# Kernel tuning notes

Hardware: AMD Instinct MI355X
Metric: run time of the kernel (lower is better)

Reference implementation:

```python
import jax, jax.numpy as jnp
import numpy as np

E = 512        # embed_dim
H = 16         # num_heads
R = 8          # num_relation_heads
NH = H - R     # num_normal_heads
HD = E // H    # head_dim
SCALING = HD ** -0.5
B, LQ, LK = 2, 2048, 2048


def setup_inputs() -> dict:
    key = jax.random.key(0)
    ks = jax.random.split(key, 14)
    s = 1.0 / np.sqrt(E)  # keep pre-softmax logits moderate so exp() is stable
    inp = {
        "query": jax.random.normal(ks[0], (B, LQ, E), jnp.float32),
        "key": jax.random.normal(ks[1], (B, LK, E), jnp.float32),
        "value": jax.random.normal(ks[2], (B, LK, E), jnp.float32),
        "relation_weights": jax.random.uniform(ks[3], (B, R, LQ, LK), jnp.float32),
        "Wq": jax.random.normal(ks[4], (E, E), jnp.float32) * s,
        "bq": jnp.zeros((E,), jnp.float32),
        "Wk": jax.random.normal(ks[5], (E, E), jnp.float32) * s,
        "bk": jnp.zeros((E,), jnp.float32),
        "Wv": jax.random.normal(ks[6], (E, E), jnp.float32) * s,
        "bv": jnp.zeros((E,), jnp.float32),
        "Wo": jax.random.normal(ks[7], (E, E), jnp.float32) * s,
        "bo": jnp.zeros((E,), jnp.float32),
        "ln_gamma": jnp.ones((E,), jnp.float32),
        "ln_beta": jnp.zeros((E,), jnp.float32),
    }
    return inp


def reference(query, key, value, relation_weights, Wq, bq, Wk, bk, Wv, bv, Wo, bo, ln_gamma, ln_beta):
    b, lq, _ = query.shape
    lk = key.shape[1]
    # projections; weights stored as [in, out] so y = x @ W + b
    q = (query @ Wq + bq).reshape(b, lq, H, HD)
    k = (key @ Wk + bk).reshape(b, lk, H, HD)
    v = (value @ Wv + bv).reshape(b, lk, H, HD)
    # scores: [B, H, Lq, Lk]
    scores = jnp.einsum("bqhd,bkhd->bhqk", q, k) * SCALING
    # normal heads: standard softmax
    normal_attn = jax.nn.softmax(scores[:, :NH], axis=-1)
    # relation heads: exp(scores) * relation_weights, renormalized
    rel = jnp.exp(scores[:, NH:]) * relation_weights
    rel = rel / (rel.sum(axis=-1, keepdims=True) + 1e-6)
    attn = jnp.concatenate([normal_attn, rel], axis=1)  # [B, H, Lq, Lk]
    # weighted values -> [B, Lq, E]
    out = jnp.einsum("bhqk,bkhd->bqhd", attn, v).reshape(b, lq, E)
    out = out @ Wo + bo
    # LayerNorm (eps=1e-5, torch default)
    mu = out.mean(axis=-1, keepdims=True)
    var = out.var(axis=-1, keepdims=True)
    out = (out - mu) * jax.lax.rsqrt(var + 1e-5) * ln_gamma + ln_beta
    return out
```

## Files before the change

### kernel.cpp

```cpp
#include <hip/hip_runtime.h>


using u16 = unsigned short;
using u32 = unsigned int;

typedef __attribute__((ext_vector_type(8))) short bf16x8;
typedef __attribute__((ext_vector_type(8))) _Float16 f16x8;
typedef __attribute__((ext_vector_type(4))) float f32x4;

#define H_  16
#define NH_ 8
#define HD_ 32
#define L_  2048
#define E_  512
#define B_  2
#define M_  4096
#define KSPLIT 2
static constexpr float QSCALE_ = 0.17677669529663689f * 1.44269504088896340f;

__device__ inline u16 f2bf(float x) {
  union { float f; u32 u; } v; v.f = x;
  u32 r = v.u + 0x7FFFu + ((v.u >> 16) & 1u);
  return (u16)(r >> 16);
}
__device__ inline float bf2f(u16 x) {
  union { u32 u; float f; } v; v.u = ((u32)x) << 16; return v.f;
}
__device__ inline u16 f2h(float x) {
  union { _Float16 h; u16 u; } v; v.h = (_Float16)x; return v.u;
}
__device__ inline float h2f(u16 x) {
  union { u16 u; _Float16 h; } v; v.u = x; return (float)v.h;
}

__global__ __launch_bounds__(256) void k_prep(const float* __restrict__ qa, const float* __restrict__ ka,
                                              const float* __restrict__ va,
                                              u16* __restrict__ oq, u16* __restrict__ ok, u16* __restrict__ ov,
                                              const float* __restrict__ Wq, const float* __restrict__ Wk,
                                              const float* __restrict__ Wv, const float* __restrict__ Wo,
                                              u16* __restrict__ Tq, u16* __restrict__ Tk,
                                              u16* __restrict__ Tv, u16* __restrict__ To) {
  __shared__ u16 tile[64][65];
  int y = blockIdx.y;
  if (y < 3) {
    const float* s = (y == 0) ? qa : (y == 1) ? ka : va;
    u16* d = (y == 0) ? oq : (y == 1) ? ok : ov;
    size_t i = ((size_t)blockIdx.x * 256 + threadIdx.x) * 4;
    float4 v = *(const float4*)(s + i);
    uint2 pk;
    pk.x = (u32)f2bf(v.x) | ((u32)f2bf(v.y) << 16);
    pk.y = (u32)f2bf(v.z) | ((u32)f2bf(v.w) << 16);
    *(uint2*)(d + i) = pk;
    return;
  }
  if (blockIdx.x >= 256) return;
  int bid = blockIdx.x;
  int z = bid >> 6, rem = bid & 63;
  int r0 = ((rem >> 3) & 7) * 64, c0 = (rem & 7) * 64;
  const float* W = (z == 0) ? Wq : (z == 1) ? Wk : (z == 2) ? Wv : Wo;
  u16* T = (z == 0) ? Tq : (z == 1) ? Tk : (z == 2) ? Tv : To;
  int tw = threadIdx.x >> 6, tl = threadIdx.x & 63;
#pragma unroll
  for (int i = 0; i < 16; ++i) {
    int r = i * 4 + tw;
    tile[r][tl] = f2bf(W[(size_t)(r0 + r) * E_ + c0 + tl]);
  }
  __syncthreads();
#pragma unroll
  for (int i = 0; i < 16; ++i) {
    int r = i * 4 + tw;
    T[(size_t)(c0 + r) * E_ + r0 + tl] = tile[tl][r];
  }
}

template <int MODE>
__device__ inline void gemm_body(const u16* __restrict__ A, const u16* __restrict__ Bt,
                                 const float* __restrict__ bias, void* __restrict__ out,
                                 const float* __restrict__ pden, float oscale, int ofmt) {
  __shared__ __align__(16) u16 smem[2 * 64 * 72];
  u16* As = smem;
  u16* Bs = smem + 64 * 72;
  const int tid = threadIdx.x;
  const int lane = tid & 63, wid = tid >> 6;
  const int m0 = blockIdx.x * 64, n0 = blockIdx.y * 64;
  const int wm = (wid >> 1) * 32, wn = (wid & 1) * 32;
  const int mrow = lane & 15, quad = lane >> 4;
  f32x4 acc[2][2] = {};
  for (int k0 = 0; k0 < 512; k0 += 64) {
    __syncthreads();
#pragma unroll
    for (int i = 0; i < 2; ++i) {
      int task = i * 256 + tid;
      int r = task >> 3, c = task & 7;
      *(uint4*)(Bs + r * 72 + c * 8) = *(const uint4*)(Bt + (size_t)(n0 + r) * 512 + k0 + c * 8);
      if (MODE == 0) {
        *(uint4*)(As + r * 72 + c * 8) = *(const uint4*)(A + (size_t)(m0 + r) * 512 + k0 + c * 8);
      } else {
        int gm = m0 + r;
        int bb = gm >> 11, q = gm & (L_ - 1);
        int e0 = k0 + c * 8;
        int hh = e0 >> 5, d = e0 & (HD_ - 1);
        size_t i0 = ((size_t)(0 * B_ + bb) * H_ + hh) * L_ + q;
        size_t i1 = ((size_t)(1 * B_ + bb) * H_ + hh) * L_ + q;
        uint4 n0v = *(const uint4*)(A + i0 * HD_ + d);
        uint4 n1v = *(const uint4*)(A + i1 * HD_ + d);
        float den = pden[i0] + pden[i1] + ((hh >= NH_) ? 1e-6f : 0.f);
        float rinv = __builtin_amdgcn_rcpf(den);
        const u16* p0 = (const u16*)&n0v;
        const u16* p1 = (const u16*)&n1v;
        u16 o8[8];
#pragma unroll
        for (int j = 0; j < 8; ++j) o8[j] = f2bf((h2f(p0[j]) + h2f(p1[j])) * rinv);
        *(uint4*)(As + r * 72 + c * 8) = *(const uint4*)o8;
      }
    }
    __syncthreads();
#pragma unroll
    for (int kk = 0; kk < 64; kk += 32) {
      bf16x8 af[2], bfr[2];
#pragma unroll
      for (int f = 0; f < 2; ++f)
        af[f] = *(const bf16x8*)(As + (wm + f * 16 + mrow) * 72 + kk + quad * 8);
#pragma unroll
      for (int f = 0; f < 2; ++f)
        bfr[f] = *(const bf16x8*)(Bs + (wn + f * 16 + mrow) * 72 + kk + quad * 8);
#pragma unroll
      for (int fm = 0; fm < 2; ++fm)
#pragma unroll
        for (int fn = 0; fn < 2; ++fn)
          acc[fm][fn] = __builtin_amdgcn_mfma_f32_16x16x32_bf16(af[fm], bfr[fn], acc[fm][fn], 0, 0, 0);
    }
  }
  if (MODE == 0) {
    __syncthreads();
    u16* wscr = smem + wid * (32 * 36);
#pragma unroll
    for (int fn = 0; fn < 2; ++fn) {
      float bv = bias[n0 + wn + fn * 16 + mrow];
#pragma unroll
      for (int fm = 0; fm < 2; ++fm)
#pragma unroll
        for (int r = 0; r < 4; ++r) {
          float x = (acc[fm][fn][r] + bv) * oscale;
          wscr[(fm * 16 + quad * 4 + r) * 36 + fn * 16 + mrow] = ofmt ? f2h(x) : f2bf(x);
        }
    }
    asm volatile("s_waitcnt lgkmcnt(0)" ::: "memory");
    const int hg = (n0 + wn) >> 5;
    const int row = lane >> 1, j = lane & 1;
    int gm = m0 + wm + row;
    int bb = gm >> 11, q = gm & (L_ - 1);
    u16* dst = (u16*)out + (((size_t)(bb * H_ + hg)) * L_ + q) * HD_ + j * 16;
    uint4 v0 = *(const uint4*)(wscr + row * 36 + j * 16);
    uint4 v1 = *(const uint4*)(wscr + row * 36 + j * 16 + 8);
    *(uint4*)dst = v0;
    *(uint4*)(dst + 8) = v1;
  } else {
#pragma unroll
    for (int fn = 0; fn < 2; ++fn) {
      int gn = n0 + wn + fn * 16 + mrow;
      float bv = bias[gn];
#pragma unroll
      for (int fm = 0; fm < 2; ++fm)
#pragma unroll
        for (int r = 0; r < 4; ++r) {
          int gm = m0 + wm + fm * 16 + quad * 4 + r;
          ((float*)out)[(size_t)gm * E_ + gn] = acc[fm][fn][r] + bv;
        }
    }
  }
}

__global__ __launch_bounds__(256) void k_gemm_qkv(const u16* Xq, const u16* Xk, const u16* Xv,
                                                  const u16* Tq, const u16* Tk, const u16* Tv,
                                                  const float* bq, const float* bk, const float* bv,
                                                  u16* Qb, u16* Kb, u16* Vb) {
  int z = blockIdx.z;
  const u16* A = (z == 0) ? Xq : (z == 1) ? Xk : Xv;
  const u16* T = (z == 0) ? Tq : (z == 1) ? Tk : Tv;
  const float* bi = (z == 0) ? bq : (z == 1) ? bk : bv;
  u16* o = (z == 0) ? Qb : (z == 1) ? Kb : Vb;
  float os = (z == 0) ? QSCALE_ : 1.0f;
  int of = (z == 2) ? 1 : 0;
  gemm_body<0>(A, T, bi, o, nullptr, os, of);
}

__global__ __launch_bounds__(256) void k_gemm_o(const u16* Pnum, const u16* T, const float* bi,
                                                float* Y, const float* Pden) {
  gemm_body<1>(Pnum, T, bi, Y, Pden, 1.0f, 0);
}

__global__ __launch_bounds__(256) void k_attn(const u16* __restrict__ Qb, const u16* __restrict__ Kb,
                                              const u16* __restrict__ Vb, const float* __restrict__ relw,
                                              u16* __restrict__ Pnum, float* __restrict__ Pden) {
  const int tid = threadIdx.x, lane = tid & 63, wid = tid >> 6;
  const int lid = blockIdx.x + 32 * blockIdx.y + 512 * blockIdx.z;
  const int xcd = lid & 7, rest = lid >> 3;
  const int qb = rest & 31, ghi = rest >> 5;
  const int g = ghi * 8 + xcd;
  const int h = g & 15, zz = g >> 4;
  const int b = zz & 1, s = zz >> 1;
  const int q0 = qb * 64;
  const int kbase = s * (L_ / KSPLIT);
  const int kend = kbase + L_ / KSPLIT;
  const bool isrel = (h >= NH_);
  const size_t headOff = ((size_t)(b * H_ + h)) * L_ * HD_;
  const float* wbase = isrel ? relw + ((size_t)(b * (H_ - NH_) + (h - NH_))) * L_ * L_ : nullptr;

  __shared__ __align__(16) u16 Qs[64 * 40];
  __shared__ __align__(16) u16 Ks[64 * 40];
  __shared__ __align__(16) u16 Vts[32 * 72];
  __shared__ __align__(16) u16 Ps[4][16 * 72];
  __shared__ __align__(16) u16 Ws[64 * 68];

  {
    int r = tid >> 2, c = tid & 3;
    *(uint4*)(Qs + r * 40 + c * 8) = *(const uint4*)(Qb + headOff + (size_t)(q0 + r) * HD_ + c * 8);
  }
  __syncthreads();
  const int mrow = lane & 15, quad = lane >> 4;
  bf16x8 qa = *(const bf16x8*)(Qs + (wid * 16 + mrow) * 40 + quad * 8);
  f32x4 accd[2] = {};
  float den[4] = {0.f, 0.f, 0.f, 0.f};

  uint4 rA, rB;
  float4 rw[4];
  const int vp = tid >> 2, vc = tid & 3;
  const int t2 = tid - 128;
  const int wq = tid >> 2, wkc = (tid & 3) * 4;

  auto LOAD = [&](int kt) {
    if (tid < 128) {
      const u16* vsrc = Vb + headOff + (size_t)(kt + 2 * vp) * HD_ + vc * 8;
      rA = *(const uint4*)(vsrc);
      rB = *(const uint4*)(vsrc + HD_);
    } else {
      int task0 = t2 * 2, task1 = t2 * 2 + 1;
      rA = *(const uint4*)(Kb + headOff + (size_t)(kt + (task0 >> 2)) * HD_ + (task0 & 3) * 8);
      rB = *(const uint4*)(Kb + headOff + (size_t)(kt + (task1 >> 2)) * HD_ + (task1 & 3) * 8);
    }
    if (isrel) {
      const float* wsrc = wbase + (size_t)(q0 + wq) * L_ + kt + wkc;
#pragma unroll
      for (int j = 0; j < 4; ++j) rw[j] = *(const float4*)(wsrc + j * 16);
    }
  };
  auto WRITE = [&]() {
    if (tid < 128) {
      const u16* s0 = (const u16*)&rA;
      const u16* s1 = (const u16*)&rB;
#pragma unroll
      for (int i = 0; i < 8; ++i) {
        u32 pk = (u32)s0[i] | ((u32)s1[i] << 16);
        *(u32*)(Vts + (vc * 8 + i) * 72 + 2 * vp) = pk;
      }
    } else {
      int task0 = t2 * 2, task1 = t2 * 2 + 1;
      *(uint4*)(Ks + (task0 >> 2) * 40 + (task0 & 3) * 8) = rA;
      *(uint4*)(Ks + (task1 >> 2) * 40 + (task1 & 3) * 8) = rB;
    }
    if (isrel) {
#pragma unroll
      for (int j = 0; j < 4; ++j) {
        uint2 pk;
        pk.x = (u32)f2bf(rw[j].x) | ((u32)f2bf(rw[j].y) << 16);
        pk.y = (u32)f2bf(rw[j].z) | ((u32)f2bf(rw[j].w) << 16);
        *(uint2*)(Ws + wq * 68 + wkc + j * 16) = pk;
      }
    }
  };

  LOAD(kbase);
  for (int kt = kbase; kt < kend; kt += 64) {
    __syncthreads();
    WRITE();
    if (kt + 64 < kend) LOAD(kt + 64);
    __syncthreads();

    u16* pw = Ps[wid];
#pragma unroll
    for (int f = 0; f < 4; ++f) {
      bf16x8 kb = *(const bf16x8*)(Ks + (f * 16 + mrow) * 40 + quad * 8);
      f32x4 z = {0.f, 0.f, 0.f, 0.f};
      f32x4 sc = __builtin_amdgcn_mfma_f32_16x16x32_bf16(qa, kb, z, 0, 0, 0);
#pragma unroll
      for (int r = 0; r < 4; ++r) {
        float e = exp2f(sc[r]);
        if (isrel)
          e *= bf2f(Ws[(wid * 16 + quad * 4 + r) * 68 + f * 16 + mrow]);
        den[r] += e;
        pw[(quad * 4 + r) * 72 + f * 16 + mrow] = f2h(e);
      }
    }
    asm volatile("s_waitcnt lgkmcnt(0)" ::: "memory");
#pragma unroll
    for (int kk = 0; kk < 2; ++kk) {
      f16x8 pa = *(const f16x8*)(pw + mrow * 72 + kk * 32 + quad * 8);
#pragma unroll
      for (int dh = 0; dh < 2; ++dh) {
        f16x8 vhf = *(const f16x8*)(Vts + (dh * 16 + mrow) * 72 + kk * 32 + quad * 8);
        accd[dh] = __builtin_amdgcn_mfma_f32_16x16x32_f16(pa, vhf, accd[dh], 0, 0, 0);
      }
    }
  }

#pragma unroll
  for (int off = 1; off < 16; off <<= 1)
#pragma unroll
    for (int r = 0; r < 4; ++r) den[r] += __shfl_xor(den[r], off, 64);

  const size_t pidx = ((size_t)(s * B_ + b) * H_ + h) * L_;
#pragma unroll
  for (int dh = 0; dh < 2; ++dh)
#pragma unroll
    for (int r = 0; r < 4; ++r) {
      int qg = q0 + wid * 16 + quad * 4 + r;
      Pnum[(pidx + qg) * HD_ + dh * 16 + mrow] = f2h(accd[dh][r]);
    }
  if (mrow == 0) {
    int qg = q0 + wid * 16 + quad * 4;
    float4 dv = {den[0], den[1], den[2], den[3]};
    *(float4*)(Pden + pidx + qg) = dv;
  }
}

__global__ __launch_bounds__(256) void k_ln(const float* __restrict__ Y, const float* __restrict__ gamma,
                                            const float* __restrict__ beta, float* __restrict__ out) {
  int row = blockIdx.x, tid = threadIdx.x;
  const float* y = Y + (size_t)row * E_;
  float2 v = *(const float2*)(y + tid * 2);
  float s = v.x + v.y, sq = v.x * v.x + v.y * v.y;
#pragma unroll
  for (int off = 1; off < 64; off <<= 1) {
    s += __shfl_xor(s, off, 64);
    sq += __shfl_xor(sq, off, 64);
  }
  __shared__ float ss[4], ssq[4];
  int wid = tid >> 6, lane = tid & 63;
  if (lane == 0) { ss[wid] = s; ssq[wid] = sq; }
  __syncthreads();
  s = ss[0] + ss[1] + ss[2] + ss[3];
  sq = ssq[0] + ssq[1] + ssq[2] + ssq[3];
  float mean = s * (1.f / E_);
  float var = sq * (1.f / E_) - mean * mean;
  float rstd = rsqrtf(var + 1e-5f);
  float2 g = *(const float2*)(gamma + tid * 2);
  float2 be = *(const float2*)(beta + tid * 2);
  float2 o;
  o.x = (v.x - mean) * rstd * g.x + be.x;
  o.y = (v.y - mean) * rstd * g.y + be.y;
  *(float2*)(out + (size_t)row * E_ + tid * 2) = o;
}

extern "C" void kernel_launch(void* const* d_in, const int* in_sizes, int n_in,
                              void* d_out, int out_size, void* d_ws, size_t ws_size,
                              hipStream_t stream) {
  const float* query = (const float*)d_in[0];
  const float* key   = (const float*)d_in[1];
  const float* value = (const float*)d_in[2];
  const float* relw  = (const float*)d_in[3];
  const float* Wq = (const float*)d_in[4];
  const float* bq = (const float*)d_in[5];
  const float* Wk = (const float*)d_in[6];
  const float* bk = (const float*)d_in[7];
  const float* Wv = (const float*)d_in[8];
  const float* bv = (const float*)d_in[9];
  const float* Wo = (const float*)d_in[10];
  const float* bo = (const float*)d_in[11];
  const float* gamma = (const float*)d_in[12];
  const float* beta  = (const float*)d_in[13];

  char* ws = (char*)d_ws;
  u16* Xq = (u16*)(ws + 0);
  u16* Xk = (u16*)(ws + 4194304);
  u16* Xv = (u16*)(ws + 8388608);
  u16* Tq = (u16*)(ws + 12582912);
  u16* Tk = (u16*)(ws + 13107200);
  u16* Tv = (u16*)(ws + 13631488);
  u16* To = (u16*)(ws + 14155776);
  u16* Qb = (u16*)(ws + 14680064);
  u16* Kb = (u16*)(ws + 18874368);
  u16* Vb = (u16*)(ws + 23068672);
  u16*   Pnum = (u16*)(ws + 0);
  float* Pden = (float*)(ws + 8388608);
  float* Y = (float*)(ws + 14680064);

  k_prep<<<dim3(2048, 4, 1), 256, 0, stream>>>(query, key, value, Xq, Xk, Xv,
                                               Wq, Wk, Wv, Wo, Tq, Tk, Tv, To);
  k_gemm_qkv<<<dim3(64, 8, 3), 256, 0, stream>>>(Xq, Xk, Xv, Tq, Tk, Tv, bq, bk, bv, Qb, Kb, Vb);
  k_attn<<<dim3(32, 16, B_ * KSPLIT), 256, 0, stream>>>(Qb, Kb, Vb, relw, Pnum, Pden);
  k_gemm_o<<<dim3(64, 8, 1), 256, 0, stream>>>(Pnum, To, bo, Y, Pden);
  k_ln<<<M_, 256, 0, stream>>>(Y, gamma, beta, (float*)d_out);
}
```

Before: 478.0 us.

## Drop split-K attention, fuse input bf16 cast into QKV GEMM, normalize in-kernel

```diff
diff --git a/kernel.cpp b/kernel.cpp
--- a/kernel.cpp
+++ b/kernel.cpp
@@ -15,7 +15,6 @@
 #define E_  512
 #define B_  2
 #define M_  4096
-#define KSPLIT 2
 static constexpr float QSCALE_ = 0.17677669529663689f * 1.44269504088896340f;
 
 __device__ inline u16 f2bf(float x) {
@@ -23,42 +22,19 @@
   u32 r = v.u + 0x7FFFu + ((v.u >> 16) & 1u);
   return (u16)(r >> 16);
 }
-__device__ inline float bf2f(u16 x) {
-  union { u32 u; float f; } v; v.u = ((u32)x) << 16; return v.f;
-}
 __device__ inline u16 f2h(float x) {
   union { _Float16 h; u16 u; } v; v.h = (_Float16)x; return v.u;
 }
-__device__ inline float h2f(u16 x) {
-  union { u16 u; _Float16 h; } v; v.u = x; return (float)v.h;
-}
-
-__global__ __launch_bounds__(256) void k_prep(const float* __restrict__ qa, const float* __restrict__ ka,
-                                              const float* __restrict__ va,
-                                              u16* __restrict__ oq, u16* __restrict__ ok, u16* __restrict__ ov,
-                                              const float* __restrict__ Wq, const float* __restrict__ Wk,
-                                              const float* __restrict__ Wv, const float* __restrict__ Wo,
-                                              u16* __restrict__ Tq, u16* __restrict__ Tk,
-                                              u16* __restrict__ Tv, u16* __restrict__ To) {
-  __shared__ u16 tile[64][65];
-  int y = blockIdx.y;
-  if (y < 3) {
-    const float* s = (y == 0) ? qa : (y == 1) ? ka : va;
-    u16* d = (y == 0) ? oq : (y == 1) ? ok : ov;
-    size_t i = ((size_t)blockIdx.x * 256 + threadIdx.x) * 4;
-    float4 v = *(const float4*)(s + i);
-    uint2 pk;
-    pk.x = (u32)f2bf(v.x) | ((u32)f2bf(v.y) << 16);
-    pk.y = (u32)f2bf(v.z) | ((u32)f2bf(v.w) << 16);
-    *(uint2*)(d + i) = pk;
-    return;
-  }
-  if (blockIdx.x >= 256) return;
-  int bid = blockIdx.x;
-  int z = bid >> 6, rem = bid & 63;
-  int r0 = ((rem >> 3) & 7) * 64, c0 = (rem & 7) * 64;
+
+__global__ __launch_bounds__(256) void k_wtrans(const float* __restrict__ Wq, const float* __restrict__ Wk,
+                                                const float* __restrict__ Wv, const float* __restrict__ Wo,
+                                                u16* __restrict__ Tq, u16* __restrict__ Tk,
+                                                u16* __restrict__ Tv, u16* __restrict__ To) {
+  int z = blockIdx.z;
   const float* W = (z == 0) ? Wq : (z == 1) ? Wk : (z == 2) ? Wv : Wo;
   u16* T = (z == 0) ? Tq : (z == 1) ? Tk : (z == 2) ? Tv : To;
+  __shared__ u16 tile[64][65];
+  int r0 = blockIdx.y * 64, c0 = blockIdx.x * 64;
   int tw = threadIdx.x >> 6, tl = threadIdx.x & 63;
 #pragma unroll
   for (int i = 0; i < 16; ++i) {
@@ -73,10 +49,10 @@
   }
 }
 
-template <int MODE>
-__device__ inline void gemm_body(const u16* __restrict__ A, const u16* __restrict__ Bt,
+template <int AF32, int EPI>
+__device__ inline void gemm_body(const void* __restrict__ A, const u16* __restrict__ Bt,
                                  const float* __restrict__ bias, void* __restrict__ out,
-                                 const float* __restrict__ pden, float oscale, int ofmt) {
+                                 float oscale, int ofmt) {
   __shared__ __align__(16) u16 smem[2 * 64 * 72];
   u16* As = smem;
   u16* Bs = smem + 64 * 72;
@@ -93,25 +69,16 @@
       int task = i * 256 + tid;
       int r = task >> 3, c = task & 7;
       *(uint4*)(Bs + r * 72 + c * 8) = *(const uint4*)(Bt + (size_t)(n0 + r) * 512 + k0 + c * 8);
-      if (MODE == 0) {
-        *(uint4*)(As + r * 72 + c * 8) = *(const uint4*)(A + (size_t)(m0 + r) * 512 + k0 + c * 8);
+      if (AF32) {
+        const float* af = (const float*)A + (size_t)(m0 + r) * 512 + k0 + c * 8;
+        float4 v0 = *(const float4*)af;
+        float4 v1 = *(const float4*)(af + 4);
+        u16 o8[8] = {f2bf(v0.x), f2bf(v0.y), f2bf(v0.z), f2bf(v0.w),
+                     f2bf(v1.x), f2bf(v1.y), f2bf(v1.z), f2bf(v1.w)};
+        *(uint4*)(As + r * 72 + c * 8) = *(const uint4*)o8;
       } else {
-        int gm = m0 + r;
-        int bb = gm >> 11, q = gm & (L_ - 1);
-        int e0 = k0 + c * 8;
-        int hh = e0 >> 5, d = e0 & (HD_ - 1);
-        size_t i0 = ((size_t)(0 * B_ + bb) * H_ + hh) * L_ + q;
-        size_t i1 = ((size_t)(1 * B_ + bb) * H_ + hh) * L_ + q;
-        uint4 n0v = *(const uint4*)(A + i0 * HD_ + d);
-        uint4 n1v = *(const uint4*)(A + i1 * HD_ + d);
-        float den = pden[i0] + pden[i1] + ((hh >= NH_) ? 1e-6f : 0.f);
-        float rinv = __builtin_amdgcn_rcpf(den);
-        const u16* p0 = (const u16*)&n0v;
-        const u16* p1 = (const u16*)&n1v;
-        u16 o8[8];
-#pragma unroll
-        for (int j = 0; j < 8; ++j) o8[j] = f2bf((h2f(p0[j]) + h2f(p1[j])) * rinv);
-        *(uint4*)(As + r * 72 + c * 8) = *(const uint4*)o8;
+        *(uint4*)(As + r * 72 + c * 8) =
+            *(const uint4*)((const u16*)A + (size_t)(m0 + r) * 512 + k0 + c * 8);
       }
     }
     __syncthreads();
@@ -131,7 +98,7 @@
           acc[fm][fn] = __builtin_amdgcn_mfma_f32_16x16x32_bf16(af[fm], bfr[fn], acc[fm][fn], 0, 0, 0);
     }
   }
-  if (MODE == 0) {
+  if (EPI == 0) {
     __syncthreads();
     u16* wscr = smem + wid * (32 * 36);
 #pragma unroll
@@ -171,65 +138,54 @@
   }
 }
 
-__global__ __launch_bounds__(256) void k_gemm_qkv(const u16* Xq, const u16* Xk, const u16* Xv,
+__global__ __launch_bounds__(256) void k_gemm_qkv(const float* Xq, const float* Xk, const float* Xv,
                                                   const u16* Tq, const u16* Tk, const u16* Tv,
                                                   const float* bq, const float* bk, const float* bv,
                                                   u16* Qb, u16* Kb, u16* Vb) {
   int z = blockIdx.z;
-  const u16* A = (z == 0) ? Xq : (z == 1) ? Xk : Xv;
+  const float* A = (z == 0) ? Xq : (z == 1) ? Xk : Xv;
   const u16* T = (z == 0) ? Tq : (z == 1) ? Tk : Tv;
   const float* bi = (z == 0) ? bq : (z == 1) ? bk : bv;
   u16* o = (z == 0) ? Qb : (z == 1) ? Kb : Vb;
   float os = (z == 0) ? QSCALE_ : 1.0f;
   int of = (z == 2) ? 1 : 0;
-  gemm_body<0>(A, T, bi, o, nullptr, os, of);
-}
-
-__global__ __launch_bounds__(256) void k_gemm_o(const u16* Pnum, const u16* T, const float* bi,
-                                                float* Y, const float* Pden) {
-  gemm_body<1>(Pnum, T, bi, Y, Pden, 1.0f, 0);
+  gemm_body<1, 0>(A, T, bi, o, os, of);
+}
+
+__global__ __launch_bounds__(256) void k_gemm_o(const u16* AO, const u16* T, const float* bi,
+                                                float* Y) {
+  gemm_body<0, 1>(AO, T, bi, Y, 1.0f, 0);
 }
 
 __global__ __launch_bounds__(256) void k_attn(const u16* __restrict__ Qb, const u16* __restrict__ Kb,
                                               const u16* __restrict__ Vb, const float* __restrict__ relw,
-                                              u16* __restrict__ Pnum, float* __restrict__ Pden) {
+                                              u16* __restrict__ AO) {
   const int tid = threadIdx.x, lane = tid & 63, wid = tid >> 6;
   const int lid = blockIdx.x + 32 * blockIdx.y + 512 * blockIdx.z;
   const int xcd = lid & 7, rest = lid >> 3;
   const int qb = rest & 31, ghi = rest >> 5;
   const int g = ghi * 8 + xcd;
-  const int h = g & 15, zz = g >> 4;
-  const int b = zz & 1, s = zz >> 1;
+  const int h = g & 15, b = g >> 4;
   const int q0 = qb * 64;
-  const int kbase = s * (L_ / KSPLIT);
-  const int kend = kbase + L_ / KSPLIT;
   const bool isrel = (h >= NH_);
   const size_t headOff = ((size_t)(b * H_ + h)) * L_ * HD_;
   const float* wbase = isrel ? relw + ((size_t)(b * (H_ - NH_) + (h - NH_))) * L_ * L_ : nullptr;
 
-  __shared__ __align__(16) u16 Qs[64 * 40];
   __shared__ __align__(16) u16 Ks[64 * 40];
   __shared__ __align__(16) u16 Vts[32 * 72];
   __shared__ __align__(16) u16 Ps[4][16 * 72];
-  __shared__ __align__(16) u16 Ws[64 * 68];
-
-  {
-    int r = tid >> 2, c = tid & 3;
-    *(uint4*)(Qs + r * 40 + c * 8) = *(const uint4*)(Qb + headOff + (size_t)(q0 + r) * HD_ + c * 8);
-  }
-  __syncthreads();
+
   const int mrow = lane & 15, quad = lane >> 4;
-  bf16x8 qa = *(const bf16x8*)(Qs + (wid * 16 + mrow) * 40 + quad * 8);
+  bf16x8 qa = *(const bf16x8*)(Qb + headOff + (size_t)(q0 + wid * 16 + mrow) * HD_ + quad * 8);
   f32x4 accd[2] = {};
   float den[4] = {0.f, 0.f, 0.f, 0.f};
 
   uint4 rA, rB;
-  float4 rw[4];
+  float rwv[16];
   const int vp = tid >> 2, vc = tid & 3;
   const int t2 = tid - 128;
-  const int wq = tid >> 2, wkc = (tid & 3) * 4;
-
-  auto LOAD = [&](int kt) {
+
+  auto LOAD_KV = [&](int kt) {
     if (tid < 128) {
       const u16* vsrc = Vb + headOff + (size_t)(kt + 2 * vp) * HD_ + vc * 8;
       rA = *(const uint4*)(vsrc);
@@ -239,10 +195,15 @@
       rA = *(const uint4*)(Kb + headOff + (size_t)(kt + (task0 >> 2)) * HD_ + (task0 & 3) * 8);
       rB = *(const uint4*)(Kb + headOff + (size_t)(kt + (task1 >> 2)) * HD_ + (task1 & 3) * 8);
     }
+  };
+  auto LOAD_REL = [&](int kt) {
     if (isrel) {
-      const float* wsrc = wbase + (size_t)(q0 + wq) * L_ + kt + wkc;
-#pragma unroll
-      for (int j = 0; j < 4; ++j) rw[j] = *(const float4*)(wsrc + j * 16);
+      const float* wsrc = wbase + (size_t)(q0 + wid * 16 + quad * 4) * L_ + kt + mrow;
+#pragma unroll
+      for (int r = 0; r < 4; ++r)
+#pragma unroll
+        for (int f = 0; f < 4; ++f)
+          rwv[r * 4 + f] = wsrc[(size_t)r * L_ + f * 16];
     }
   };
   auto WRITE = [&]() {
@@ -259,22 +220,14 @@
       *(uint4*)(Ks + (task0 >> 2) * 40 + (task0 & 3) * 8) = rA;
       *(uint4*)(Ks + (task1 >> 2) * 40 + (task1 & 3) * 8) = rB;
     }
-    if (isrel) {
-#pragma unroll
-      for (int j = 0; j < 4; ++j) {
-        uint2 pk;
-        pk.x = (u32)f2bf(rw[j].x) | ((u32)f2bf(rw[j].y) << 16);
-        pk.y = (u32)f2bf(rw[j].z) | ((u32)f2bf(rw[j].w) << 16);
-        *(uint2*)(Ws + wq * 68 + wkc + j * 16) = pk;
-      }
-    }
   };
 
-  LOAD(kbase);
-  for (int kt = kbase; kt < kend; kt += 64) {
+  LOAD_KV(0);
+  LOAD_REL(0);
+  for (int kt = 0; kt < L_; kt += 64) {
     __syncthreads();
     WRITE();
-    if (kt + 64 < kend) LOAD(kt + 64);
+    if (kt + 64 < L_) LOAD_KV(kt + 64);
     __syncthreads();
 
     u16* pw = Ps[wid];
@@ -287,11 +240,12 @@
       for (int r = 0; r < 4; ++r) {
         float e = exp2f(sc[r]);
         if (isrel)
-          e *= bf2f(Ws[(wid * 16 + quad * 4 + r) * 68 + f * 16 + mrow]);
+          e *= rwv[r * 4 + f];
         den[r] += e;
         pw[(quad * 4 + r) * 72 + f * 16 + mrow] = f2h(e);
       }
     }
+    if (kt + 64 < L_) LOAD_REL(kt + 64);
     asm volatile("s_waitcnt lgkmcnt(0)" ::: "memory");
 #pragma unroll
     for (int kk = 0; kk < 2; ++kk) {
@@ -309,19 +263,22 @@
 #pragma unroll
     for (int r = 0; r < 4; ++r) den[r] += __shfl_xor(den[r], off, 64);
 
-  const size_t pidx = ((size_t)(s * B_ + b) * H_ + h) * L_;
+  float rinv[4];
+#pragma unroll
+  for (int r = 0; r < 4; ++r)
+    rinv[r] = __builtin_amdgcn_rcpf(den[r] + (isrel ? 1e-6f : 0.f));
+
+  u16* pw = Ps[wid];
 #pragma unroll
   for (int dh = 0; dh < 2; ++dh)
 #pragma unroll
-    for (int r = 0; r < 4; ++r) {
-      int qg = q0 + wid * 16 + quad * 4 + r;
-      Pnum[(pidx + qg) * HD_ + dh * 16 + mrow] = f2h(accd[dh][r]);
-    }
-  if (mrow == 0) {
-    int qg = q0 + wid * 16 + quad * 4;
-    float4 dv = {den[0], den[1], den[2], den[3]};
-    *(float4*)(Pden + pidx + qg) = dv;
-  }
+    for (int r = 0; r < 4; ++r)
+      pw[(quad * 4 + r) * 72 + dh * 16 + mrow] = f2bf(accd[dh][r] * rinv[r]);
+  asm volatile("s_waitcnt lgkmcnt(0)" ::: "memory");
+  const int row = lane >> 2, j = lane & 3;
+  const int qg = q0 + wid * 16 + row;
+  *(uint4*)(AO + ((size_t)(b * L_ + qg)) * E_ + h * HD_ + j * 8) =
+      *(const uint4*)(pw + row * 72 + j * 8);
 }
 
 __global__ __launch_bounds__(256) void k_ln(const float* __restrict__ Y, const float* __restrict__ gamma,
@@ -371,24 +328,20 @@
   const float* beta  = (const float*)d_in[13];
 
   char* ws = (char*)d_ws;
-  u16* Xq = (u16*)(ws + 0);
-  u16* Xk = (u16*)(ws + 4194304);
-  u16* Xv = (u16*)(ws + 8388608);
-  u16* Tq = (u16*)(ws + 12582912);
-  u16* Tk = (u16*)(ws + 13107200);
-  u16* Tv = (u16*)(ws + 13631488);
-  u16* To = (u16*)(ws + 14155776);
-  u16* Qb = (u16*)(ws + 14680064);
-  u16* Kb = (u16*)(ws + 18874368);
-  u16* Vb = (u16*)(ws + 23068672);
-  u16*   Pnum = (u16*)(ws + 0);
-  float* Pden = (float*)(ws + 8388608);
-  float* Y = (float*)(ws + 14680064);
-
-  k_prep<<<dim3(2048, 4, 1), 256, 0, stream>>>(query, key, value, Xq, Xk, Xv,
-                                               Wq, Wk, Wv, Wo, Tq, Tk, Tv, To);
-  k_gemm_qkv<<<dim3(64, 8, 3), 256, 0, stream>>>(Xq, Xk, Xv, Tq, Tk, Tv, bq, bk, bv, Qb, Kb, Vb);
-  k_attn<<<dim3(32, 16, B_ * KSPLIT), 256, 0, stream>>>(Qb, Kb, Vb, relw, Pnum, Pden);
-  k_gemm_o<<<dim3(64, 8, 1), 256, 0, stream>>>(Pnum, To, bo, Y, Pden);
+  u16* Tq = (u16*)(ws + 0);
+  u16* Tk = (u16*)(ws + 524288);
+  u16* Tv = (u16*)(ws + 1048576);
+  u16* To = (u16*)(ws + 1572864);
+  u16* Qb = (u16*)(ws + 2097152);
+  u16* Kb = (u16*)(ws + 6291456);
+  u16* Vb = (u16*)(ws + 10485760);
+  u16* AO = (u16*)(ws + 14680064);
+  float* Y = (float*)(ws + 18874368);
+
+  k_wtrans<<<dim3(8, 8, 4), 256, 0, stream>>>(Wq, Wk, Wv, Wo, Tq, Tk, Tv, To);
+  k_gemm_qkv<<<dim3(64, 8, 3), 256, 0, stream>>>(query, key, value, Tq, Tk, Tv,
+                                                 bq, bk, bv, Qb, Kb, Vb);
+  k_attn<<<dim3(32, 16, 2), 256, 0, stream>>>(Qb, Kb, Vb, relw, AO);
+  k_gemm_o<<<dim3(64, 8, 1), 256, 0, stream>>>(AO, To, bo, Y);
   k_ln<<<M_, 256, 0, stream>>>(Y, gamma, beta, (float*)d_out);
 }
```

New measurement: 453.3 us. -5.2%, faster.
